# Kernel optimization log

Hardware: AMD Instinct MI355X
Metric: run time of the kernel (lower is better)

The kernel has to match this reference:

```python
import jax, jax.numpy as jnp
import numpy as np

B, N, G, K, V = 4, 512, 8, 64, 32000


def setup_inputs() -> dict:
    key = jax.random.key(0)
    k1, k2, k3 = jax.random.split(key, 3)
    phi = jax.random.normal(k1, (B, N, G, K), dtype=jnp.float32)
    # psi initialized uniform(-0.5, 0.5) as in torch.nn.init.uniform_
    psi = jax.random.uniform(k2, (V, K), dtype=jnp.float32, minval=-0.5, maxval=0.5)
    # perm[h, v] = index of h^{-1} acting on vocab word v (data-dependent permutation)
    perm = jax.random.randint(k3, (G, V), 0, V, dtype=jnp.int64)
    return {"phi": phi, "psi": psi, "perm": perm}


def reference(phi, psi, perm):
    # For each group element h: logits[b,n,v] += dot(phi[b,n,h,:], psi[perm[h,v],:])
    # Gather psi rows per group element: [G, V, K]
    psi_g = psi[perm]
    logits = jnp.einsum("bnhk,hvk->bnv", phi, psi_g)  # [B, N, V]
    return jax.nn.softmax(logits, axis=-1)
```

## Files before the change

### kernel.cpp

```cpp
#include <hip/hip_runtime.h>
#include <math.h>


#define M_ROWS 2048
#define V_DIM  32000
#define C_DIM  512
#define G_DIM  8
#define K_DIM  64
#define BM     128
#define BV     128
#define BK     32
#define NVBLK  (V_DIM / BV)
#define LDS_ROW 40

typedef _Float16 f16x8 __attribute__((ext_vector_type(8)));
typedef _Float16 f16x4 __attribute__((ext_vector_type(4)));
typedef float    f32x4 __attribute__((ext_vector_type(4)));

__global__ __launch_bounds__(256, 2) void gdecode_gemm(
    const float* __restrict__ phi, const float* __restrict__ psi,
    const int* __restrict__ perm, const int pstride,
    float* __restrict__ out, float* __restrict__ smax, float* __restrict__ ssum)
{
  __shared__ __align__(16) _Float16 lds[3 * BM * LDS_ROW];
  _Float16* sAhi = lds;
  _Float16* sAlo = lds + BM * LDS_ROW;
  _Float16* sB   = lds + 2 * BM * LDS_ROW;

  const int t     = threadIdx.x;
  const int vbase = blockIdx.x * BV;
  const int mbase = blockIdx.y * BM;

  const int kg = t & 7;
  const int r0 = t >> 3;

  const int wid  = t >> 6;
  const int lane = t & 63;
  const int wm   = wid & 1;
  const int wv   = wid >> 1;
  const int lrow = lane & 15;
  const int quad = lane >> 4;

  f32x4 acc[4][4] = {};

  for (int it = 0; it < 16; ++it) {
    const int cb  = it * BK;
    const int h   = cb >> 6;
    const int kin = cb & 63;

    float4 av[4], bv[4];
    #pragma unroll
    for (int i = 0; i < 4; ++i) {
      int m = r0 + i * 32;
      av[i] = *(const float4*)(phi + (size_t)(mbase + m) * C_DIM + cb + kg * 4);
    }
    #pragma unroll
    for (int i = 0; i < 4; ++i) {
      int v  = r0 + i * 32;
      int pr = perm[(size_t)(h * V_DIM + vbase + v) * pstride];
      bv[i]  = *(const float4*)(psi + (size_t)pr * K_DIM + kin + kg * 4);
    }

    __syncthreads();

    #pragma unroll
    for (int i = 0; i < 4; ++i) {
      int m = r0 + i * 32;
      float4 x = av[i];
      _Float16 h0 = (_Float16)x.x, h1 = (_Float16)x.y,
               h2 = (_Float16)x.z, h3 = (_Float16)x.w;
      f16x4 hi = {h0, h1, h2, h3};
      f16x4 lo = {(_Float16)(x.x - (float)h0), (_Float16)(x.y - (float)h1),
                  (_Float16)(x.z - (float)h2), (_Float16)(x.w - (float)h3)};
      *(f16x4*)(sAhi + m * LDS_ROW + kg * 4) = hi;
      *(f16x4*)(sAlo + m * LDS_ROW + kg * 4) = lo;
    }
    #pragma unroll
    for (int i = 0; i < 4; ++i) {
      int v = r0 + i * 32;
      float4 x = bv[i];
      f16x4 w = {(_Float16)x.x, (_Float16)x.y, (_Float16)x.z, (_Float16)x.w};
      *(f16x4*)(sB + v * LDS_ROW + kg * 4) = w;
    }

    __syncthreads();

    f16x8 ah[4], al[4], bf[4];
    #pragma unroll
    for (int i = 0; i < 4; ++i) {
      ah[i] = *(const f16x8*)(sAhi + (wm * 64 + i * 16 + lrow) * LDS_ROW + quad * 8);
      al[i] = *(const f16x8*)(sAlo + (wm * 64 + i * 16 + lrow) * LDS_ROW + quad * 8);
      bf[i] = *(const f16x8*)(sB   + (wv * 64 + i * 16 + lrow) * LDS_ROW + quad * 8);
    }
    #pragma unroll
    for (int i = 0; i < 4; ++i) {
      #pragma unroll
      for (int j = 0; j < 4; ++j) {
        acc[i][j] = __builtin_amdgcn_mfma_f32_16x16x32_f16(ah[i], bf[j], acc[i][j], 0, 0, 0);
        acc[i][j] = __builtin_amdgcn_mfma_f32_16x16x32_f16(al[i], bf[j], acc[i][j], 0, 0, 0);
      }
    }
  }

  __syncthreads();
  float* redmax = (float*)lds;
  float* redsum = redmax + 2 * BM;
  const int rowb = wm * 64;

  #pragma unroll
  for (int i = 0; i < 4; ++i) {
    #pragma unroll
    for (int r = 0; r < 4; ++r) {
      float v = fmaxf(fmaxf(acc[i][0][r], acc[i][1][r]),
                      fmaxf(acc[i][2][r], acc[i][3][r]));
      v = fmaxf(v, __shfl_xor(v, 1));
      v = fmaxf(v, __shfl_xor(v, 2));
      v = fmaxf(v, __shfl_xor(v, 4));
      v = fmaxf(v, __shfl_xor(v, 8));
      if (lrow == 0) redmax[(rowb + i * 16 + quad * 4 + r) * 2 + wv] = v;
    }
  }
  __syncthreads();
  float gmx[4][4];
  #pragma unroll
  for (int i = 0; i < 4; ++i) {
    #pragma unroll
    for (int r = 0; r < 4; ++r) {
      int row = rowb + i * 16 + quad * 4 + r;
      gmx[i][r] = fmaxf(redmax[row * 2], redmax[row * 2 + 1]);
    }
  }
  #pragma unroll
  for (int i = 0; i < 4; ++i) {
    #pragma unroll
    for (int r = 0; r < 4; ++r) {
      float s = __expf(acc[i][0][r] - gmx[i][r]) + __expf(acc[i][1][r] - gmx[i][r])
              + __expf(acc[i][2][r] - gmx[i][r]) + __expf(acc[i][3][r] - gmx[i][r]);
      s += __shfl_xor(s, 1);
      s += __shfl_xor(s, 2);
      s += __shfl_xor(s, 4);
      s += __shfl_xor(s, 8);
      if (lrow == 0) redsum[(rowb + i * 16 + quad * 4 + r) * 2 + wv] = s;
    }
  }
  __syncthreads();
  if (smax != nullptr && t < BM) {
    int row = t;
    size_t o = (size_t)(mbase + row) * NVBLK + blockIdx.x;
    smax[o] = fmaxf(redmax[row * 2], redmax[row * 2 + 1]);
    ssum[o] = redsum[row * 2] + redsum[row * 2 + 1];
  }
  #pragma unroll
  for (int i = 0; i < 4; ++i) {
    #pragma unroll
    for (int j = 0; j < 4; ++j) {
      #pragma unroll
      for (int r = 0; r < 4; ++r) {
        int grow = mbase + rowb + i * 16 + quad * 4 + r;
        int gcol = vbase + wv * 64 + j * 16 + lrow;
        out[(size_t)grow * V_DIM + gcol] = acc[i][j][r];
      }
    }
  }
}

__global__ __launch_bounds__(256) void gdecode_softmax_ws(
    float* __restrict__ out, const float* __restrict__ smax, const float* __restrict__ ssum)
{
  __shared__ float sbuf[4];
  const int m = blockIdx.x;
  const int t = threadIdx.x;
  const float* rm = smax + (size_t)m * NVBLK;
  const float* rs = ssum + (size_t)m * NVBLK;

  float lm = -3.4e38f;
  for (int i = t; i < NVBLK; i += 256) lm = fmaxf(lm, rm[i]);
  for (int d = 1; d < 64; d <<= 1) lm = fmaxf(lm, __shfl_xor(lm, d));
  if ((t & 63) == 0) sbuf[t >> 6] = lm;
  __syncthreads();
  const float M = fmaxf(fmaxf(sbuf[0], sbuf[1]), fmaxf(sbuf[2], sbuf[3]));
  __syncthreads();

  float ls = 0.f;
  for (int i = t; i < NVBLK; i += 256) ls += rs[i] * __expf(rm[i] - M);
  for (int d = 1; d < 64; d <<= 1) ls += __shfl_xor(ls, d);
  if ((t & 63) == 0) sbuf[t >> 6] = ls;
  __syncthreads();
  const float inv = 1.f / (sbuf[0] + sbuf[1] + sbuf[2] + sbuf[3]);

  float4* row = (float4*)(out + (size_t)m * V_DIM);
  for (int i = t; i < V_DIM / 4; i += 256) {
    float4 x = row[i];
    x.x = __expf(x.x - M) * inv;
    x.y = __expf(x.y - M) * inv;
    x.z = __expf(x.z - M) * inv;
    x.w = __expf(x.w - M) * inv;
    row[i] = x;
  }
}

__global__ __launch_bounds__(256) void gdecode_softmax_nows(float* __restrict__ out)
{
  __shared__ float sbuf[4];
  const int m = blockIdx.x;
  const int t = threadIdx.x;
  float4* row = (float4*)(out + (size_t)m * V_DIM);

  float lm = -3.4e38f;
  for (int i = t; i < V_DIM / 4; i += 256) {
    float4 x = row[i];
    lm = fmaxf(lm, fmaxf(fmaxf(x.x, x.y), fmaxf(x.z, x.w)));
  }
  for (int d = 1; d < 64; d <<= 1) lm = fmaxf(lm, __shfl_xor(lm, d));
  if ((t & 63) == 0) sbuf[t >> 6] = lm;
  __syncthreads();
  const float M = fmaxf(fmaxf(sbuf[0], sbuf[1]), fmaxf(sbuf[2], sbuf[3]));
  __syncthreads();

  float ls = 0.f;
  for (int i = t; i < V_DIM / 4; i += 256) {
    float4 x = row[i];
    ls += __expf(x.x - M) + __expf(x.y - M) + __expf(x.z - M) + __expf(x.w - M);
  }
  for (int d = 1; d < 64; d <<= 1) ls += __shfl_xor(ls, d);
  if ((t & 63) == 0) sbuf[t >> 6] = ls;
  __syncthreads();
  const float inv = 1.f / (sbuf[0] + sbuf[1] + sbuf[2] + sbuf[3]);

  for (int i = t; i < V_DIM / 4; i += 256) {
    float4 x = row[i];
    x.x = __expf(x.x - M) * inv;
    x.y = __expf(x.y - M) * inv;
    x.z = __expf(x.z - M) * inv;
    x.w = __expf(x.w - M) * inv;
    row[i] = x;
  }
}

extern "C" void kernel_launch(void* const* d_in, const int* in_sizes, int n_in,
                              void* d_out, int out_size, void* d_ws, size_t ws_size,
                              hipStream_t stream)
{
  const float* phi  = (const float*)d_in[0];
  const float* psi  = (const float*)d_in[1];
  const int*   perm = (const int*)d_in[2];
  const int pstride = (in_sizes[2] == 2 * G_DIM * V_DIM) ? 2 : 1;

  float* out = (float*)d_out;

  const size_t need = (size_t)M_ROWS * NVBLK * 2 * sizeof(float);
  const bool hasws = (d_ws != nullptr) && (ws_size >= need);
  float* smax = hasws ? (float*)d_ws : nullptr;
  float* ssum = hasws ? smax + (size_t)M_ROWS * NVBLK : nullptr;

  dim3 grid(NVBLK, M_ROWS / BM);
  gdecode_gemm<<<grid, 256, 0, stream>>>(phi, psi, perm, pstride, out, smax, ssum);

  if (hasws)
    gdecode_softmax_ws<<<M_ROWS, 256, 0, stream>>>(out, smax, ssum);
  else
    gdecode_softmax_nows<<<M_ROWS, 256, 0, stream>>>(out);
}
```

Measured before the change: 553.6 us.

## Pre-convert operands to fp16 and load MFMA fragments directly from global memory

Adds pre-pass kernels that convert psi to fp16 and split phi into fp16 hi/lo parts in workspace. The GEMM then loads MFMA fragments straight from global memory with no LDS staging or per-tile barriers, and raises occupancy to 3 blocks per SM. The softmax is split into a per-row stats kernel and a 2D-grid scale kernel for more parallelism. The cost is extra launches and workspace traffic, plus direct global reads of the fp16 operands that rely on cache for reuse.

```diff
diff --git a/kernel.cpp b/kernel.cpp
--- a/kernel.cpp
+++ b/kernel.cpp
@@ -17,10 +17,199 @@
 typedef _Float16 f16x4 __attribute__((ext_vector_type(4)));
 typedef float    f32x4 __attribute__((ext_vector_type(4)));
 
-__global__ __launch_bounds__(256, 2) void gdecode_gemm(
+
+__global__ __launch_bounds__(256) void conv_psi(const float* __restrict__ psi,
+                                                _Float16* __restrict__ psi16)
+{
+  int i = blockIdx.x * 256 + threadIdx.x;
+  float4 x = ((const float4*)psi)[i];
+  f16x4 w = {(_Float16)x.x, (_Float16)x.y, (_Float16)x.z, (_Float16)x.w};
+  *(f16x4*)(psi16 + (size_t)i * 4) = w;
+}
+
+__global__ __launch_bounds__(256) void conv_phi(const float* __restrict__ phi,
+                                                _Float16* __restrict__ phiH,
+                                                _Float16* __restrict__ phiL)
+{
+  int i = blockIdx.x * 256 + threadIdx.x;
+  float4 x = ((const float4*)phi)[i];
+  _Float16 h0 = (_Float16)x.x, h1 = (_Float16)x.y, h2 = (_Float16)x.z, h3 = (_Float16)x.w;
+  f16x4 hi = {h0, h1, h2, h3};
+  f16x4 lo = {(_Float16)(x.x - (float)h0), (_Float16)(x.y - (float)h1),
+              (_Float16)(x.z - (float)h2), (_Float16)(x.w - (float)h3)};
+  *(f16x4*)(phiH + (size_t)i * 4) = hi;
+  *(f16x4*)(phiL + (size_t)i * 4) = lo;
+}
+
+
+__global__ __launch_bounds__(256, 3) void gdecode_gemm_direct(
+    const _Float16* __restrict__ phiH, const _Float16* __restrict__ phiL,
+    const _Float16* __restrict__ psi16, const int* __restrict__ perm, const int pstride,
+    float* __restrict__ out, float* __restrict__ smax, float* __restrict__ ssum)
+{
+  __shared__ float red[4 * BM];
+  float* redmax = red;
+  float* redsum = red + 2 * BM;
+
+  const int t     = threadIdx.x;
+  const int vbase = blockIdx.x * BV;
+  const int mbase = blockIdx.y * BM;
+  const int wid   = t >> 6;
+  const int lane  = t & 63;
+  const int wm    = wid & 1;
+  const int wv    = wid >> 1;
+  const int lrow  = lane & 15;
+  const int quad  = lane >> 4;
+
+  f32x4 acc[4][4] = {};
+
+  const int arow0 = mbase + wm * 64 + lrow;
+  const _Float16* pH = phiH + (size_t)arow0 * C_DIM + quad * 8;
+  const _Float16* pL = phiL + (size_t)arow0 * C_DIM + quad * 8;
+  const int vcol0 = vbase + wv * 64 + lrow;
+
+  #pragma unroll
+  for (int h = 0; h < 8; ++h) {
+    int pr[4];
+    #pragma unroll
+    for (int j = 0; j < 4; ++j)
+      pr[j] = perm[(size_t)(h * V_DIM + vcol0 + j * 16) * pstride];
+
+    #pragma unroll
+    for (int half = 0; half < 2; ++half) {
+      const int cb = h * 64 + half * 32;
+      f16x8 ah[4], al[4], bf[4];
+      #pragma unroll
+      for (int i = 0; i < 4; ++i) {
+        ah[i] = *(const f16x8*)(pH + (size_t)i * 16 * C_DIM + cb);
+        al[i] = *(const f16x8*)(pL + (size_t)i * 16 * C_DIM + cb);
+      }
+      #pragma unroll
+      for (int j = 0; j < 4; ++j)
+        bf[j] = *(const f16x8*)(psi16 + (size_t)pr[j] * K_DIM + half * 32 + quad * 8);
+
+      #pragma unroll
+      for (int i = 0; i < 4; ++i) {
+        #pragma unroll
+        for (int j = 0; j < 4; ++j) {
+          acc[i][j] = __builtin_amdgcn_mfma_f32_16x16x32_f16(ah[i], bf[j], acc[i][j], 0, 0, 0);
+          acc[i][j] = __builtin_amdgcn_mfma_f32_16x16x32_f16(al[i], bf[j], acc[i][j], 0, 0, 0);
+        }
+      }
+    }
+  }
+
+  const int rowb = wm * 64;
+  #pragma unroll
+  for (int i = 0; i < 4; ++i) {
+    #pragma unroll
+    for (int r = 0; r < 4; ++r) {
+      float v = fmaxf(fmaxf(acc[i][0][r], acc[i][1][r]),
+                      fmaxf(acc[i][2][r], acc[i][3][r]));
+      v = fmaxf(v, __shfl_xor(v, 1));
+      v = fmaxf(v, __shfl_xor(v, 2));
+      v = fmaxf(v, __shfl_xor(v, 4));
+      v = fmaxf(v, __shfl_xor(v, 8));
+      if (lrow == 0) redmax[(rowb + i * 16 + quad * 4 + r) * 2 + wv] = v;
+    }
+  }
+  __syncthreads();
+  float gmx[4][4];
+  #pragma unroll
+  for (int i = 0; i < 4; ++i) {
+    #pragma unroll
+    for (int r = 0; r < 4; ++r) {
+      int row = rowb + i * 16 + quad * 4 + r;
+      gmx[i][r] = fmaxf(redmax[row * 2], redmax[row * 2 + 1]);
+    }
+  }
+  #pragma unroll
+  for (int i = 0; i < 4; ++i) {
+    #pragma unroll
+    for (int r = 0; r < 4; ++r) {
+      float s = __expf(acc[i][0][r] - gmx[i][r]) + __expf(acc[i][1][r] - gmx[i][r])
+              + __expf(acc[i][2][r] - gmx[i][r]) + __expf(acc[i][3][r] - gmx[i][r]);
+      s += __shfl_xor(s, 1);
+      s += __shfl_xor(s, 2);
+      s += __shfl_xor(s, 4);
+      s += __shfl_xor(s, 8);
+      if (lrow == 0) redsum[(rowb + i * 16 + quad * 4 + r) * 2 + wv] = s;
+    }
+  }
+  __syncthreads();
+  if (t < BM) {
+    int row = t;
+    size_t o = (size_t)(mbase + row) * NVBLK + blockIdx.x;
+    smax[o] = fmaxf(redmax[row * 2], redmax[row * 2 + 1]);
+    ssum[o] = redsum[row * 2] + redsum[row * 2 + 1];
+  }
+  #pragma unroll
+  for (int i = 0; i < 4; ++i) {
+    #pragma unroll
+    for (int j = 0; j < 4; ++j) {
+      #pragma unroll
+      for (int r = 0; r < 4; ++r) {
+        int grow = mbase + rowb + i * 16 + quad * 4 + r;
+        int gcol = vbase + wv * 64 + j * 16 + lrow;
+        out[(size_t)grow * V_DIM + gcol] = acc[i][j][r];
+      }
+    }
+  }
+}
+
+
+__global__ __launch_bounds__(256) void gdecode_stats(
+    const float* __restrict__ smax, const float* __restrict__ ssum,
+    float* __restrict__ rowM, float* __restrict__ rowInv)
+{
+  __shared__ float sbuf[4];
+  __shared__ float sM;
+  const int m = blockIdx.x;
+  const int t = threadIdx.x;
+  const float* rm = smax + (size_t)m * NVBLK;
+  const float* rs = ssum + (size_t)m * NVBLK;
+
+  float lm = -3.4e38f;
+  for (int i = t; i < NVBLK; i += 256) lm = fmaxf(lm, rm[i]);
+  for (int d = 1; d < 64; d <<= 1) lm = fmaxf(lm, __shfl_xor(lm, d));
+  if ((t & 63) == 0) sbuf[t >> 6] = lm;
+  __syncthreads();
+  if (t == 0) sM = fmaxf(fmaxf(sbuf[0], sbuf[1]), fmaxf(sbuf[2], sbuf[3]));
+  __syncthreads();
+  const float M = sM;
+
+  float ls = 0.f;
+  for (int i = t; i < NVBLK; i += 256) ls += rs[i] * __expf(rm[i] - M);
+  for (int d = 1; d < 64; d <<= 1) ls += __shfl_xor(ls, d);
+  if ((t & 63) == 0) sbuf[t >> 6] = ls;
+  __syncthreads();
+  if (t == 0) {
+    rowM[m]   = M;
+    rowInv[m] = 1.f / (sbuf[0] + sbuf[1] + sbuf[2] + sbuf[3]);
+  }
+}
+
+__global__ __launch_bounds__(256) void gdecode_scale(
+    float* __restrict__ out, const float* __restrict__ rowM, const float* __restrict__ rowInv)
+{
+  const int m  = blockIdx.y;
+  const int c4 = blockIdx.x * 256 + threadIdx.x;
+  if (c4 >= V_DIM / 4) return;
+  const float M   = rowM[m];
+  const float inv = rowInv[m];
+  float4* row = (float4*)(out + (size_t)m * V_DIM);
+  float4 x = row[c4];
+  x.x = __expf(x.x - M) * inv;
+  x.y = __expf(x.y - M) * inv;
+  x.z = __expf(x.z - M) * inv;
+  x.w = __expf(x.w - M) * inv;
+  row[c4] = x;
+}
+
+
+__global__ __launch_bounds__(256, 2) void gdecode_gemm_lds(
     const float* __restrict__ phi, const float* __restrict__ psi,
-    const int* __restrict__ perm, const int pstride,
-    float* __restrict__ out, float* __restrict__ smax, float* __restrict__ ssum)
+    const int* __restrict__ perm, const int pstride, float* __restrict__ out)
 {
   __shared__ __align__(16) _Float16 lds[3 * BM * LDS_ROW];
   _Float16* sAhi = lds;
@@ -30,10 +219,8 @@
   const int t     = threadIdx.x;
   const int vbase = blockIdx.x * BV;
   const int mbase = blockIdx.y * BM;
-
   const int kg = t & 7;
   const int r0 = t >> 3;
-
   const int wid  = t >> 6;
   const int lane = t & 63;
   const int wm   = wid & 1;
@@ -50,19 +237,15 @@
 
     float4 av[4], bv[4];
     #pragma unroll
-    for (int i = 0; i < 4; ++i) {
-      int m = r0 + i * 32;
-      av[i] = *(const float4*)(phi + (size_t)(mbase + m) * C_DIM + cb + kg * 4);
-    }
-    #pragma unroll
-    for (int i = 0; i < 4; ++i) {
-      int v  = r0 + i * 32;
-      int pr = perm[(size_t)(h * V_DIM + vbase + v) * pstride];
+    for (int i = 0; i < 4; ++i)
+      av[i] = *(const float4*)(phi + (size_t)(mbase + r0 + i * 32) * C_DIM + cb + kg * 4);
+    #pragma unroll
+    for (int i = 0; i < 4; ++i) {
+      int pr = perm[(size_t)(h * V_DIM + vbase + r0 + i * 32) * pstride];
       bv[i]  = *(const float4*)(psi + (size_t)pr * K_DIM + kin + kg * 4);
     }
 
     __syncthreads();
-
     #pragma unroll
     for (int i = 0; i < 4; ++i) {
       int m = r0 + i * 32;
@@ -77,12 +260,10 @@
     }
     #pragma unroll
     for (int i = 0; i < 4; ++i) {
-      int v = r0 + i * 32;
       float4 x = bv[i];
       f16x4 w = {(_Float16)x.x, (_Float16)x.y, (_Float16)x.z, (_Float16)x.w};
-      *(f16x4*)(sB + v * LDS_ROW + kg * 4) = w;
-    }
-
+      *(f16x4*)(sB + (r0 + i * 32) * LDS_ROW + kg * 4) = w;
+    }
     __syncthreads();
 
     f16x8 ah[4], al[4], bf[4];
@@ -102,61 +283,13 @@
     }
   }
 
-  __syncthreads();
-  float* redmax = (float*)lds;
-  float* redsum = redmax + 2 * BM;
-  const int rowb = wm * 64;
-
-  #pragma unroll
-  for (int i = 0; i < 4; ++i) {
-    #pragma unroll
-    for (int r = 0; r < 4; ++r) {
-      float v = fmaxf(fmaxf(acc[i][0][r], acc[i][1][r]),
-                      fmaxf(acc[i][2][r], acc[i][3][r]));
-      v = fmaxf(v, __shfl_xor(v, 1));
-      v = fmaxf(v, __shfl_xor(v, 2));
-      v = fmaxf(v, __shfl_xor(v, 4));
-      v = fmaxf(v, __shfl_xor(v, 8));
-      if (lrow == 0) redmax[(rowb + i * 16 + quad * 4 + r) * 2 + wv] = v;
-    }
-  }
-  __syncthreads();
-  float gmx[4][4];
-  #pragma unroll
-  for (int i = 0; i < 4; ++i) {
-    #pragma unroll
-    for (int r = 0; r < 4; ++r) {
-      int row = rowb + i * 16 + quad * 4 + r;
-      gmx[i][r] = fmaxf(redmax[row * 2], redmax[row * 2 + 1]);
-    }
-  }
-  #pragma unroll
-  for (int i = 0; i < 4; ++i) {
-    #pragma unroll
-    for (int r = 0; r < 4; ++r) {
-      float s = __expf(acc[i][0][r] - gmx[i][r]) + __expf(acc[i][1][r] - gmx[i][r])
-              + __expf(acc[i][2][r] - gmx[i][r]) + __expf(acc[i][3][r] - gmx[i][r]);
-      s += __shfl_xor(s, 1);
-      s += __shfl_xor(s, 2);
-      s += __shfl_xor(s, 4);
-      s += __shfl_xor(s, 8);
-      if (lrow == 0) redsum[(rowb + i * 16 + quad * 4 + r) * 2 + wv] = s;
-    }
-  }
-  __syncthreads();
-  if (smax != nullptr && t < BM) {
-    int row = t;
-    size_t o = (size_t)(mbase + row) * NVBLK + blockIdx.x;
-    smax[o] = fmaxf(redmax[row * 2], redmax[row * 2 + 1]);
-    ssum[o] = redsum[row * 2] + redsum[row * 2 + 1];
-  }
   #pragma unroll
   for (int i = 0; i < 4; ++i) {
     #pragma unroll
     for (int j = 0; j < 4; ++j) {
       #pragma unroll
       for (int r = 0; r < 4; ++r) {
-        int grow = mbase + rowb + i * 16 + quad * 4 + r;
+        int grow = mbase + wm * 64 + i * 16 + quad * 4 + r;
         int gcol = vbase + wv * 64 + j * 16 + lrow;
         out[(size_t)grow * V_DIM + gcol] = acc[i][j][r];
       }
@@ -164,31 +297,38 @@
   }
 }
 
-__global__ __launch_bounds__(256) void gdecode_softmax_ws(
-    float* __restrict__ out, const float* __restrict__ smax, const float* __restrict__ ssum)
+__global__ __launch_bounds__(256) void gdecode_softmax_nows(float* __restrict__ out)
 {
   __shared__ float sbuf[4];
+  __shared__ float sM, sInv;
   const int m = blockIdx.x;
   const int t = threadIdx.x;
-  const float* rm = smax + (size_t)m * NVBLK;
-  const float* rs = ssum + (size_t)m * NVBLK;
+  float4* row = (float4*)(out + (size_t)m * V_DIM);
 
   float lm = -3.4e38f;
-  for (int i = t; i < NVBLK; i += 256) lm = fmaxf(lm, rm[i]);
+  for (int i = t; i < V_DIM / 4; i += 256) {
+    float4 x = row[i];
+    lm = fmaxf(lm, fmaxf(fmaxf(x.x, x.y), fmaxf(x.z, x.w)));
+  }
   for (int d = 1; d < 64; d <<= 1) lm = fmaxf(lm, __shfl_xor(lm, d));
   if ((t & 63) == 0) sbuf[t >> 6] = lm;
   __syncthreads();
-  const float M = fmaxf(fmaxf(sbuf[0], sbuf[1]), fmaxf(sbuf[2], sbuf[3]));
-  __syncthreads();
+  if (t == 0) sM = fmaxf(fmaxf(sbuf[0], sbuf[1]), fmaxf(sbuf[2], sbuf[3]));
+  __syncthreads();
+  const float M = sM;
 
   float ls = 0.f;
-  for (int i = t; i < NVBLK; i += 256) ls += rs[i] * __expf(rm[i] - M);
+  for (int i = t; i < V_DIM / 4; i += 256) {
+    float4 x = row[i];
+    ls += __expf(x.x - M) + __expf(x.y - M) + __expf(x.z - M) + __expf(x.w - M);
+  }
   for (int d = 1; d < 64; d <<= 1) ls += __shfl_xor(ls, d);
   if ((t & 63) == 0) sbuf[t >> 6] = ls;
   __syncthreads();
-  const float inv = 1.f / (sbuf[0] + sbuf[1] + sbuf[2] + sbuf[3]);
-
-  float4* row = (float4*)(out + (size_t)m * V_DIM);
+  if (t == 0) sInv = 1.f / (sbuf[0] + sbuf[1] + sbuf[2] + sbuf[3]);
+  __syncthreads();
+  const float inv = sInv;
+
   for (int i = t; i < V_DIM / 4; i += 256) {
     float4 x = row[i];
     x.x = __expf(x.x - M) * inv;
@@ -199,43 +339,6 @@
   }
 }
 
-__global__ __launch_bounds__(256) void gdecode_softmax_nows(float* __restrict__ out)
-{
-  __shared__ float sbuf[4];
-  const int m = blockIdx.x;
-  const int t = threadIdx.x;
-  float4* row = (float4*)(out + (size_t)m * V_DIM);
-
-  float lm = -3.4e38f;
-  for (int i = t; i < V_DIM / 4; i += 256) {
-    float4 x = row[i];
-    lm = fmaxf(lm, fmaxf(fmaxf(x.x, x.y), fmaxf(x.z, x.w)));
-  }
-  for (int d = 1; d < 64; d <<= 1) lm = fmaxf(lm, __shfl_xor(lm, d));
-  if ((t & 63) == 0) sbuf[t >> 6] = lm;
-  __syncthreads();
-  const float M = fmaxf(fmaxf(sbuf[0], sbuf[1]), fmaxf(sbuf[2], sbuf[3]));
-  __syncthreads();
-
-  float ls = 0.f;
-  for (int i = t; i < V_DIM / 4; i += 256) {
-    float4 x = row[i];
-    ls += __expf(x.x - M) + __expf(x.y - M) + __expf(x.z - M) + __expf(x.w - M);
-  }
-  for (int d = 1; d < 64; d <<= 1) ls += __shfl_xor(ls, d);
-  if ((t & 63) == 0) sbuf[t >> 6] = ls;
-  __syncthreads();
-  const float inv = 1.f / (sbuf[0] + sbuf[1] + sbuf[2] + sbuf[3]);
-
-  for (int i = t; i < V_DIM / 4; i += 256) {
-    float4 x = row[i];
-    x.x = __expf(x.x - M) * inv;
-    x.y = __expf(x.y - M) * inv;
-    x.z = __expf(x.z - M) * inv;
-    x.w = __expf(x.w - M) * inv;
-    row[i] = x;
-  }
-}
 
 extern "C" void kernel_launch(void* const* d_in, const int* in_sizes, int n_in,
                               void* d_out, int out_size, void* d_ws, size_t ws_size,
@@ -245,19 +348,39 @@
   const float* psi  = (const float*)d_in[1];
   const int*   perm = (const int*)d_in[2];
   const int pstride = (in_sizes[2] == 2 * G_DIM * V_DIM) ? 2 : 1;
-
   float* out = (float*)d_out;
 
-  const size_t need = (size_t)M_ROWS * NVBLK * 2 * sizeof(float);
-  const bool hasws = (d_ws != nullptr) && (ws_size >= need);
-  float* smax = hasws ? (float*)d_ws : nullptr;
-  float* ssum = hasws ? smax + (size_t)M_ROWS * NVBLK : nullptr;
-
-  dim3 grid(NVBLK, M_ROWS / BM);
-  gdecode_gemm<<<grid, 256, 0, stream>>>(phi, psi, perm, pstride, out, smax, ssum);
-
-  if (hasws)
-    gdecode_softmax_ws<<<M_ROWS, 256, 0, stream>>>(out, smax, ssum);
-  else
+  const size_t off_psi16 = 0;
+  const size_t off_phiH  = off_psi16 + (size_t)V_DIM * K_DIM * 2;
+  const size_t off_phiL  = off_phiH + (size_t)M_ROWS * C_DIM * 2;
+  const size_t off_smax  = off_phiL + (size_t)M_ROWS * C_DIM * 2;
+  const size_t off_ssum  = off_smax + (size_t)M_ROWS * NVBLK * 4;
+  const size_t off_rowM  = off_ssum + (size_t)M_ROWS * NVBLK * 4;
+  const size_t off_rowI  = off_rowM + (size_t)M_ROWS * 4;
+  const size_t need      = off_rowI + (size_t)M_ROWS * 4;
+
+  if (d_ws != nullptr && ws_size >= need) {
+    char* ws = (char*)d_ws;
+    _Float16* psi16 = (_Float16*)(ws + off_psi16);
+    _Float16* phiH  = (_Float16*)(ws + off_phiH);
+    _Float16* phiL  = (_Float16*)(ws + off_phiL);
+    float* smax   = (float*)(ws + off_smax);
+    float* ssum   = (float*)(ws + off_ssum);
+    float* rowM   = (float*)(ws + off_rowM);
+    float* rowInv = (float*)(ws + off_rowI);
+
+    conv_psi<<<(V_DIM * K_DIM / 4) / 256, 256, 0, stream>>>(psi, psi16);
+    conv_phi<<<(M_ROWS * C_DIM / 4) / 256, 256, 0, stream>>>(phi, phiH, phiL);
+
+    dim3 grid(NVBLK, M_ROWS / BM);
+    gdecode_gemm_direct<<<grid, 256, 0, stream>>>(phiH, phiL, psi16, perm, pstride,
+                                                  out, smax, ssum);
+    gdecode_stats<<<M_ROWS, 256, 0, stream>>>(smax, ssum, rowM, rowInv);
+    dim3 sgrid((V_DIM / 4 + 255) / 256, M_ROWS);
+    gdecode_scale<<<sgrid, 256, 0, stream>>>(out, rowM, rowInv);
+  } else {
+    dim3 grid(NVBLK, M_ROWS / BM);
+    gdecode_gemm_lds<<<grid, 256, 0, stream>>>(phi, psi, perm, pstride, out);
     gdecode_softmax_nows<<<M_ROWS, 256, 0, stream>>>(out);
-}
+  }
+}
```

Result: slower. 701.2 us (+26.7%).
